# Performance work log

Hardware: AMD Instinct MI355X
Metric: run time of the kernel (lower is better)

Reference implementation:

```python
import jax, jax.numpy as jnp
import numpy as np

EPS_LEN = 1e-20
EPS_DENOM = 1e-6


def _dot(a, b):
    return jnp.sum(a * b, axis=-1, keepdims=True)


def _safe_normalize(x):
    return x / jnp.sqrt(jnp.maximum(_dot(x, x), EPS_LEN))


def _auto_normals(positions, faces):
    i0, i1, i2 = faces[:, 0], faces[:, 1], faces[:, 2]
    v0 = positions[i0]
    v1 = positions[i1]
    v2 = positions[i2]
    face_normals = jnp.cross(v1 - v0, v2 - v0)  # [F,3]
    v_nrm = jnp.zeros_like(positions)
    v_nrm = v_nrm.at[i0].add(face_normals)
    v_nrm = v_nrm.at[i1].add(face_normals)
    v_nrm = v_nrm.at[i2].add(face_normals)
    default = jnp.array([0.0, 0.0, 1.0], dtype=positions.dtype)
    v_nrm = jnp.where(_dot(v_nrm, v_nrm) > EPS_LEN, v_nrm, default)
    return _safe_normalize(v_nrm)


def _compute_tangents(positions, normals, faces, texcoords, uv_faces):
    pos = [positions[faces[:, i]] for i in range(3)]
    tex = [texcoords[uv_faces[:, i]] for i in range(3)]
    uve1 = tex[1] - tex[0]
    uve2 = tex[2] - tex[0]
    pe1 = pos[1] - pos[0]
    pe2 = pos[2] - pos[0]
    nom = pe1 * uve2[..., 1:2] - pe2 * uve1[..., 1:2]  # [F,3]
    denom = uve1[..., 0:1] * uve2[..., 1:2] - uve1[..., 1:2] * uve2[..., 0:1]
    denom = jnp.where(denom > 0.0,
                      jnp.maximum(denom, EPS_DENOM),
                      jnp.minimum(denom, -EPS_DENOM))
    tang = nom / denom  # [F,3]
    tangents = jnp.zeros_like(normals)
    for i in range(3):
        tangents = tangents.at[faces[:, i]].add(tang)
    tangents = _safe_normalize(tangents)
    tangents = _safe_normalize(tangents - _dot(tangents, normals) * normals)
    return tangents


def setup_inputs() -> dict:
    key = jax.random.key(0)
    k1, k2, k3, k4 = jax.random.split(key, 4)
    V, T, F = 2_000_000, 2_200_000, 4_000_000
    positions = jax.random.normal(k1, (V, 3), dtype=jnp.float32)
    faces = jax.random.randint(k2, (F, 3), 0, V, dtype=jnp.int32)
    texcoords = jax.random.uniform(k3, (T, 2), dtype=jnp.float32)
    uv_faces = jax.random.randint(k4, (F, 3), 0, T, dtype=jnp.int32)
    return {"positions": positions, "faces": faces,
            "texcoords": texcoords, "uv_faces": uv_faces}


def reference(positions, faces, texcoords, uv_faces):
    normals = _auto_normals(positions, faces)
    tangents = _compute_tangents(positions, normals, faces, texcoords, uv_faces)
    return jnp.stack([normals, tangents])  # [2, V, 3]
```

## Files before the change

### kernel.cpp

```cpp
#include <hip/hip_runtime.h>

#define EPS_LEN   1e-20f
#define EPS_DENOM 1e-6f

#define CB_LOG   11
#define CB       (1 << CB_LOG)
#define BLKA     1024
#define MAXB     1024
#define NCHUNK   2
#define CAPC     6528

#define CB2_LOG  13
#define CB2      (1 << CB2_LOG)
#define MAXB2    256
#define CAP2     57344
#define FST      6
#define QLOG     11
#define QSIZE    (1 << QLOG)

__global__ __launch_bounds__(BLKA)
void vg_face_bin_c(const float* __restrict__ pos, const int* __restrict__ faces,
                   const float* __restrict__ tex, const int* __restrict__ uvf,
                   float* __restrict__ en, float* __restrict__ et,
                   unsigned short* __restrict__ ev,
                   int* __restrict__ cursors, int* __restrict__ validw,
                   float* __restrict__ nacc, float* __restrict__ tacc,
                   int f0, int f1, int NBC)
{
    __shared__ int h[MAXB], sc[MAXB], loff[MAXB], lfill[MAXB], gbase[MAXB];
    __shared__ float spnx[BLKA], spny[BLKA], spnz[BLKA];
    __shared__ float sptx[BLKA], spty[BLKA], sptz[BLKA];
    __shared__ unsigned short sfl[3 * BLKA];
    __shared__ unsigned short svloc[3 * BLKA];
    __shared__ unsigned short sbuck[3 * BLKA];

    const int t = threadIdx.x;
    const int f = f0 + blockIdx.x * BLKA + t;

    h[t] = 0; lfill[t] = 0;
    for (int i = t; i < 3 * BLKA; i += BLKA) sbuck[i] = 0xFFFFu;
    __syncthreads();

    const bool on = (f < f1);
    int i0 = 0, i1 = 0, i2 = 0;
    float nx = 0, ny = 0, nz = 0, txv = 0, tyv = 0, tzv = 0;

    if (on) {
        i0 = faces[3 * f + 0]; i1 = faces[3 * f + 1]; i2 = faces[3 * f + 2];

        const float p0x = pos[3*i0+0], p0y = pos[3*i0+1], p0z = pos[3*i0+2];
        const float p1x = pos[3*i1+0], p1y = pos[3*i1+1], p1z = pos[3*i1+2];
        const float p2x = pos[3*i2+0], p2y = pos[3*i2+1], p2z = pos[3*i2+2];

        const float e1x = p1x - p0x, e1y = p1y - p0y, e1z = p1z - p0z;
        const float e2x = p2x - p0x, e2y = p2y - p0y, e2z = p2z - p0z;

        nx = e1y * e2z - e1z * e2y;
        ny = e1z * e2x - e1x * e2z;
        nz = e1x * e2y - e1y * e2x;

        const int t0 = uvf[3 * f + 0];
        const int t1 = uvf[3 * f + 1];
        const int t2 = uvf[3 * f + 2];

        const float u0x = tex[2*t0+0], u0y = tex[2*t0+1];
        const float u1x = tex[2*t1+0], u1y = tex[2*t1+1];
        const float u2x = tex[2*t2+0], u2y = tex[2*t2+1];

        const float d1x = u1x - u0x, d1y = u1y - u0y;
        const float d2x = u2x - u0x, d2y = u2y - u0y;

        float denom = d1x * d2y - d1y * d2x;
        denom = (denom > 0.0f) ? fmaxf(denom, EPS_DENOM) : fminf(denom, -EPS_DENOM);
        const float inv = 1.0f / denom;

        txv = (e1x * d2y - e2x * d1y) * inv;
        tyv = (e1y * d2y - e2y * d1y) * inv;
        tzv = (e1z * d2y - e2z * d1y) * inv;

        spnx[t] = nx;  spny[t] = ny;  spnz[t] = nz;
        sptx[t] = txv; spty[t] = tyv; sptz[t] = tzv;

        atomicAdd(&h[i0 >> CB_LOG], 1);
        atomicAdd(&h[i1 >> CB_LOG], 1);
        atomicAdd(&h[i2 >> CB_LOG], 1);
    }
    __syncthreads();

    sc[t] = h[t];
    __syncthreads();
    for (int d = 1; d < MAXB; d <<= 1) {
        const int v2 = sc[t] + ((t >= d) ? sc[t - d] : 0);
        __syncthreads();
        sc[t] = v2;
        __syncthreads();
    }
    {
        loff[t] = sc[t] - h[t];
        const int cnt = h[t];
        int gb = -1;
        if (t < NBC && cnt > 0) {
            gb = atomicAdd(&cursors[t], cnt);
            if (gb + cnt <= CAPC) atomicMax(&validw[t], gb + cnt);
            else gb = -1;
        }
        gbase[t] = gb;
    }
    __syncthreads();

    if (on) {
        const int vi[3] = { i0, i1, i2 };
#pragma unroll
        for (int c = 0; c < 3; ++c) {
            const int v = vi[c];
            const int b = v >> CB_LOG;
            if (gbase[b] >= 0) {
                const int slot = atomicAdd(&lfill[b], 1);
                const int p = loff[b] + slot;
                sfl[p]   = (unsigned short)t;
                svloc[p] = (unsigned short)(v & (CB - 1));
                sbuck[p] = (unsigned short)b;
            } else {
                atomicAdd(&nacc[3*v+0], nx);
                atomicAdd(&nacc[3*v+1], ny);
                atomicAdd(&nacc[3*v+2], nz);
                atomicAdd(&tacc[3*v+0], txv);
                atomicAdd(&tacc[3*v+1], tyv);
                atomicAdd(&tacc[3*v+2], tzv);
            }
        }
    }
    __syncthreads();

    for (int i = t; i < 3 * BLKA; i += BLKA) {
        const unsigned b = sbuck[i];
        if (b != 0xFFFFu) {
            const int g = gbase[b] + (i - loff[b]);
            const size_t s = (size_t)b * CAPC + g;
            const int fl = sfl[i];
            en[s*3+0] = spnx[fl]; en[s*3+1] = spny[fl]; en[s*3+2] = spnz[fl];
            et[s*3+0] = sptx[fl]; et[s*3+1] = spty[fl]; et[s*3+2] = sptz[fl];
            ev[s] = svloc[i];
        }
    }
}

__global__ __launch_bounds__(BLKA)
void vg_reduce_c(const float* __restrict__ en, const float* __restrict__ et,
                 const unsigned short* __restrict__ ev,
                 const int* __restrict__ validw,
                 float* __restrict__ nacc, float* __restrict__ tacc,
                 int V, int isFinal)
{
    __shared__ float accn[CB * 3];
    __shared__ float acct[CB * 3];
    const int b = blockIdx.x;
    const int t = threadIdx.x;

    for (int i = t; i < CB * 3; i += BLKA) { accn[i] = 0.0f; acct[i] = 0.0f; }
    __syncthreads();

    int count = validw[b];
    if (count > CAPC) count = CAPC;
    const size_t ebase = (size_t)b * CAPC;

    for (int e = t; e < count; e += BLKA) {
        const int vloc = (int)ev[ebase + e];
        const float* pn = &en[(ebase + e) * 3];
        const float* pt = &et[(ebase + e) * 3];
        float* an = &accn[vloc * 3];
        float* at = &acct[vloc * 3];
        atomicAdd(an + 0, pn[0]);
        atomicAdd(an + 1, pn[1]);
        atomicAdd(an + 2, pn[2]);
        atomicAdd(at + 0, pt[0]);
        atomicAdd(at + 1, pt[1]);
        atomicAdd(at + 2, pt[2]);
    }
    __syncthreads();

    const int vbase = b << CB_LOG;
#pragma unroll
    for (int k = 0; k < CB; k += BLKA) {
        const int i = t + k;
        const int v = vbase + i;
        if (v < V) {
            float nx = nacc[3*v+0] + accn[3*i+0];
            float ny = nacc[3*v+1] + accn[3*i+1];
            float nz = nacc[3*v+2] + accn[3*i+2];
            float tx = tacc[3*v+0] + acct[3*i+0];
            float ty = tacc[3*v+1] + acct[3*i+1];
            float tz = tacc[3*v+2] + acct[3*i+2];

            if (isFinal) {
                const float nd = nx*nx + ny*ny + nz*nz;
                if (nd > EPS_LEN) {
                    const float invn = 1.0f / sqrtf(nd);
                    nx *= invn; ny *= invn; nz *= invn;
                } else {
                    nx = 0.0f; ny = 0.0f; nz = 1.0f;
                }

                const float td = tx*tx + ty*ty + tz*tz;
                const float invt = 1.0f / sqrtf(fmaxf(td, EPS_LEN));
                tx *= invt; ty *= invt; tz *= invt;

                const float dp = tx*nx + ty*ny + tz*nz;
                tx -= dp * nx; ty -= dp * ny; tz -= dp * nz;

                const float td2 = tx*tx + ty*ty + tz*tz;
                const float invt2 = 1.0f / sqrtf(fmaxf(td2, EPS_LEN));
                tx *= invt2; ty *= invt2; tz *= invt2;
            }

            nacc[3*v+0] = nx; nacc[3*v+1] = ny; nacc[3*v+2] = nz;
            tacc[3*v+0] = tx; tacc[3*v+1] = ty; tacc[3*v+2] = tz;
        }
    }
}

__global__ __launch_bounds__(BLKA)
void vg_face_bin3(const float* __restrict__ pos, const int* __restrict__ faces,
                  const float* __restrict__ tex, const int* __restrict__ uvf,
                  float* __restrict__ face_data,
                  unsigned* __restrict__ ef, unsigned short* __restrict__ ev,
                  int* __restrict__ cursors, int* __restrict__ validw,
                  float* __restrict__ nacc, float* __restrict__ tacc,
                  int F, int NBC)
{
    __shared__ int h[MAXB2], sc[MAXB2], loff[MAXB2], lfill[MAXB2], gbase[MAXB2];
    __shared__ unsigned       sface[3 * BLKA];
    __shared__ unsigned short svloc[3 * BLKA];
    __shared__ unsigned char  sbuck[3 * BLKA];

    const int t = threadIdx.x;
    const int f = blockIdx.x * BLKA + t;

    if (t < MAXB2) { h[t] = 0; lfill[t] = 0; }
    for (int i = t; i < 3 * BLKA; i += BLKA) sbuck[i] = 0xFF;
    __syncthreads();

    const bool on = (f < F);
    int i0 = 0, i1 = 0, i2 = 0;
    float nx = 0, ny = 0, nz = 0, txv = 0, tyv = 0, tzv = 0;

    if (on) {
        i0 = faces[3 * f + 0]; i1 = faces[3 * f + 1]; i2 = faces[3 * f + 2];

        const float p0x = pos[3*i0+0], p0y = pos[3*i0+1], p0z = pos[3*i0+2];
        const float p1x = pos[3*i1+0], p1y = pos[3*i1+1], p1z = pos[3*i1+2];
        const float p2x = pos[3*i2+0], p2y = pos[3*i2+1], p2z = pos[3*i2+2];

        const float e1x = p1x - p0x, e1y = p1y - p0y, e1z = p1z - p0z;
        const float e2x = p2x - p0x, e2y = p2y - p0y, e2z = p2z - p0z;

        nx = e1y * e2z - e1z * e2y;
        ny = e1z * e2x - e1x * e2z;
        nz = e1x * e2y - e1y * e2x;

        const int t0 = uvf[3 * f + 0];
        const int t1 = uvf[3 * f + 1];
        const int t2 = uvf[3 * f + 2];

        const float u0x = tex[2*t0+0], u0y = tex[2*t0+1];
        const float u1x = tex[2*t1+0], u1y = tex[2*t1+1];
        const float u2x = tex[2*t2+0], u2y = tex[2*t2+1];

        const float d1x = u1x - u0x, d1y = u1y - u0y;
        const float d2x = u2x - u0x, d2y = u2y - u0y;

        float denom = d1x * d2y - d1y * d2x;
        denom = (denom > 0.0f) ? fmaxf(denom, EPS_DENOM) : fminf(denom, -EPS_DENOM);
        const float inv = 1.0f / denom;

        txv = (e1x * d2y - e2x * d1y) * inv;
        tyv = (e1y * d2y - e2y * d1y) * inv;
        tzv = (e1z * d2y - e2z * d1y) * inv;

        float* fd = &face_data[(size_t)f * FST];
        reinterpret_cast<float2*>(fd)[0] = make_float2(nx, ny);
        reinterpret_cast<float2*>(fd)[1] = make_float2(nz, txv);
        reinterpret_cast<float2*>(fd)[2] = make_float2(tyv, tzv);

        atomicAdd(&h[i0 >> CB2_LOG], 1);
        atomicAdd(&h[i1 >> CB2_LOG], 1);
        atomicAdd(&h[i2 >> CB2_LOG], 1);
    }
    __syncthreads();

    if (t < MAXB2) sc[t] = h[t];
    __syncthreads();
    for (int d = 1; d < MAXB2; d <<= 1) {
        int v2 = 0;
        if (t < MAXB2) v2 = sc[t] + ((t >= d) ? sc[t - d] : 0);
        __syncthreads();
        if (t < MAXB2) sc[t] = v2;
        __syncthreads();
    }
    if (t < MAXB2) {
        loff[t] = sc[t] - h[t];
        const int cnt = h[t];
        int gb = -1;
        if (t < NBC && cnt > 0) {
            gb = atomicAdd(&cursors[t], cnt);
            if (gb + cnt <= CAP2) atomicMax(&validw[t], gb + cnt);
            else gb = -1;
        }
        gbase[t] = gb;
    }
    __syncthreads();

    if (on) {
        const int vi[3] = { i0, i1, i2 };
#pragma unroll
        for (int c = 0; c < 3; ++c) {
            const int v = vi[c];
            const int b = v >> CB2_LOG;
            if (gbase[b] >= 0) {
                const int slot = atomicAdd(&lfill[b], 1);
                const int p = loff[b] + slot;
                sface[p] = (unsigned)f;
                svloc[p] = (unsigned short)(v & (CB2 - 1));
                sbuck[p] = (unsigned char)b;
            } else {
                atomicAdd(&nacc[3*v+0], nx);
                atomicAdd(&nacc[3*v+1], ny);
                atomicAdd(&nacc[3*v+2], nz);
                atomicAdd(&tacc[3*v+0], txv);
                atomicAdd(&tacc[3*v+1], tyv);
                atomicAdd(&tacc[3*v+2], tzv);
            }
        }
    }
    __syncthreads();

    for (int i = t; i < 3 * BLKA; i += BLKA) {
        const unsigned b = sbuck[i];
        if (b != 0xFFu) {
            const int g = gbase[b] + (i - loff[b]);
            const size_t base = (size_t)b * CAP2;
            ef[base + g] = sface[i];
            ev[base + g] = svloc[i];
        }
    }
}

__global__ __launch_bounds__(BLKA)
void vg_bucket_reduce3(const float* __restrict__ face_data,
                       const unsigned* __restrict__ ef,
                       const unsigned short* __restrict__ ev,
                       const int* __restrict__ validw,
                       float* __restrict__ nacc, float* __restrict__ tacc,
                       int V)
{
    __shared__ float acc[QSIZE * 6];
    const int b = blockIdx.x;
    const int t = threadIdx.x;
    int count = validw[b];
    if (count > CAP2) count = CAP2;
    const size_t ebase = (size_t)b * CAP2;
    const int vbase = b << CB2_LOG;

    for (int q = 0; q < 4; ++q) {
        for (int i = t; i < QSIZE * 6; i += BLKA) acc[i] = 0.0f;
        __syncthreads();

        for (int e = t; e < count; e += BLKA) {
            const int vloc = (int)ev[ebase + e];
            if ((vloc >> QLOG) == q) {
                const unsigned f = ef[ebase + e];
                const float* fd = &face_data[(size_t)f * FST];
                const float2 a0 = reinterpret_cast<const float2*>(fd)[0];
                const float2 a1 = reinterpret_cast<const float2*>(fd)[1];
                const float2 a2 = reinterpret_cast<const float2*>(fd)[2];
                float* a = &acc[(vloc & (QSIZE - 1)) * 6];
                atomicAdd(a + 0, a0.x);
                atomicAdd(a + 1, a0.y);
                atomicAdd(a + 2, a1.x);
                atomicAdd(a + 3, a1.y);
                atomicAdd(a + 4, a2.x);
                atomicAdd(a + 5, a2.y);
            }
        }
        __syncthreads();

        for (int i = t; i < QSIZE; i += BLKA) {
            const int v = vbase + (q << QLOG) + i;
            if (v < V) {
                float nx = nacc[3*v+0] + acc[i*6+0];
                float ny = nacc[3*v+1] + acc[i*6+1];
                float nz = nacc[3*v+2] + acc[i*6+2];
                float tx = tacc[3*v+0] + acc[i*6+3];
                float ty = tacc[3*v+1] + acc[i*6+4];
                float tz = tacc[3*v+2] + acc[i*6+5];

                const float nd = nx*nx + ny*ny + nz*nz;
                if (nd > EPS_LEN) {
                    const float invn = 1.0f / sqrtf(nd);
                    nx *= invn; ny *= invn; nz *= invn;
                } else {
                    nx = 0.0f; ny = 0.0f; nz = 1.0f;
                }

                const float td = tx*tx + ty*ty + tz*tz;
                const float invt = 1.0f / sqrtf(fmaxf(td, EPS_LEN));
                tx *= invt; ty *= invt; tz *= invt;

                const float dp = tx*nx + ty*ny + tz*nz;
                tx -= dp * nx; ty -= dp * ny; tz -= dp * nz;

                const float td2 = tx*tx + ty*ty + tz*tz;
                const float invt2 = 1.0f / sqrtf(fmaxf(td2, EPS_LEN));
                tx *= invt2; ty *= invt2; tz *= invt2;

                nacc[3*v+0] = nx; nacc[3*v+1] = ny; nacc[3*v+2] = nz;
                tacc[3*v+0] = tx; tacc[3*v+1] = ty; tacc[3*v+2] = tz;
            }
        }
        __syncthreads();
    }
}

__global__ void vg_face_kernel(const float* __restrict__ pos,
                               const int*   __restrict__ faces,
                               const float* __restrict__ tex,
                               const int*   __restrict__ uvf,
                               float* __restrict__ nacc,
                               float* __restrict__ tacc,
                               int F) {
    int f = blockIdx.x * blockDim.x + threadIdx.x;
    if (f >= F) return;

    const int i0 = faces[3*f+0], i1 = faces[3*f+1], i2 = faces[3*f+2];

    const float p0x = pos[3*i0+0], p0y = pos[3*i0+1], p0z = pos[3*i0+2];
    const float p1x = pos[3*i1+0], p1y = pos[3*i1+1], p1z = pos[3*i1+2];
    const float p2x = pos[3*i2+0], p2y = pos[3*i2+1], p2z = pos[3*i2+2];

    const float e1x = p1x - p0x, e1y = p1y - p0y, e1z = p1z - p0z;
    const float e2x = p2x - p0x, e2y = p2y - p0y, e2z = p2z - p0z;

    const float nx = e1y*e2z - e1z*e2y;
    const float ny = e1z*e2x - e1x*e2z;
    const float nz = e1x*e2y - e1y*e2x;

    const int t0 = uvf[3*f+0], t1 = uvf[3*f+1], t2 = uvf[3*f+2];

    const float u0x = tex[2*t0+0], u0y = tex[2*t0+1];
    const float u1x = tex[2*t1+0], u1y = tex[2*t1+1];
    const float u2x = tex[2*t2+0], u2y = tex[2*t2+1];

    const float d1x = u1x - u0x, d1y = u1y - u0y;
    const float d2x = u2x - u0x, d2y = u2y - u0y;

    float denom = d1x * d2y - d1y * d2x;
    denom = (denom > 0.0f) ? fmaxf(denom, EPS_DENOM) : fminf(denom, -EPS_DENOM);
    const float inv = 1.0f / denom;

    const float tx = (e1x*d2y - e2x*d1y) * inv;
    const float ty = (e1y*d2y - e2y*d1y) * inv;
    const float tz = (e1z*d2y - e2z*d1y) * inv;

    atomicAdd(&nacc[3*i0+0], nx); atomicAdd(&nacc[3*i0+1], ny); atomicAdd(&nacc[3*i0+2], nz);
    atomicAdd(&nacc[3*i1+0], nx); atomicAdd(&nacc[3*i1+1], ny); atomicAdd(&nacc[3*i1+2], nz);
    atomicAdd(&nacc[3*i2+0], nx); atomicAdd(&nacc[3*i2+1], ny); atomicAdd(&nacc[3*i2+2], nz);
    atomicAdd(&tacc[3*i0+0], tx); atomicAdd(&tacc[3*i0+1], ty); atomicAdd(&tacc[3*i0+2], tz);
    atomicAdd(&tacc[3*i1+0], tx); atomicAdd(&tacc[3*i1+1], ty); atomicAdd(&tacc[3*i1+2], tz);
    atomicAdd(&tacc[3*i2+0], tx); atomicAdd(&tacc[3*i2+1], ty); atomicAdd(&tacc[3*i2+2], tz);
}

__global__ void vg_finalize_kernel(float* __restrict__ nacc,
                                   float* __restrict__ tacc,
                                   int V) {
    int v = blockIdx.x * blockDim.x + threadIdx.x;
    if (v >= V) return;

    float nx = nacc[3*v+0], ny = nacc[3*v+1], nz = nacc[3*v+2];
    float nd = nx*nx + ny*ny + nz*nz;
    if (nd > EPS_LEN) {
        const float invn = 1.0f / sqrtf(nd);
        nx *= invn; ny *= invn; nz *= invn;
    } else {
        nx = 0.0f; ny = 0.0f; nz = 1.0f;
    }

    float tx = tacc[3*v+0], ty = tacc[3*v+1], tz = tacc[3*v+2];
    float td = tx*tx + ty*ty + tz*tz;
    float invt = 1.0f / sqrtf(fmaxf(td, EPS_LEN));
    tx *= invt; ty *= invt; tz *= invt;
    const float dp = tx*nx + ty*ny + tz*nz;
    tx -= dp*nx; ty -= dp*ny; tz -= dp*nz;
    float td2 = tx*tx + ty*ty + tz*tz;
    float invt2 = 1.0f / sqrtf(fmaxf(td2, EPS_LEN));
    tx *= invt2; ty *= invt2; tz *= invt2;

    nacc[3*v+0] = nx; nacc[3*v+1] = ny; nacc[3*v+2] = nz;
    tacc[3*v+0] = tx; tacc[3*v+1] = ty; tacc[3*v+2] = tz;
}

extern "C" void kernel_launch(void* const* d_in, const int* in_sizes, int n_in,
                              void* d_out, int out_size, void* d_ws, size_t ws_size,
                              hipStream_t stream) {
    const float* pos   = (const float*)d_in[0];
    const int*   faces = (const int*)  d_in[1];
    const float* tex   = (const float*)d_in[2];
    const int*   uvf   = (const int*)  d_in[3];

    const int V = in_sizes[0] / 3;
    const int F = in_sizes[1] / 3;

    float* out  = (float*)d_out;
    float* nacc = out;
    float* tacc = out + (size_t)3 * V;

    hipMemsetAsync(d_out, 0, (size_t)out_size * sizeof(float), stream);

    const int NBC1 = (V + CB - 1) >> CB_LOG;
    {
        const size_t NE1   = (size_t)NBC1 * CAPC;
        const size_t en_b  = (NE1 * 12 + 255) & ~(size_t)255;
        const size_t et_b  = (NE1 * 12 + 255) & ~(size_t)255;
        const size_t ev_b  = (NE1 * 2 + 255) & ~(size_t)255;
        const size_t cur_b = ((size_t)NBC1 * sizeof(int) + 255) & ~(size_t)255;
        const size_t need1 = en_b + et_b + ev_b + 2 * cur_b + 256;

        if (ws_size >= need1 && NBC1 <= MAXB) {
            char* ws = (char*)d_ws;
            float*          en  = (float*)ws;          ws += en_b;
            float*          et  = (float*)ws;          ws += et_b;
            unsigned short* ev  = (unsigned short*)ws; ws += ev_b;
            int*            cursors = (int*)ws;        ws += cur_b;
            int*            validw  = (int*)ws;

            const int Fc = (F + NCHUNK - 1) / NCHUNK;
            for (int c = 0; c < NCHUNK; ++c) {
                const int f0 = c * Fc;
                const int f1 = (f0 + Fc < F) ? (f0 + Fc) : F;
                if (f0 >= f1) continue;

                hipMemsetAsync(cursors, 0, cur_b, stream);
                hipMemsetAsync(validw,  0, cur_b, stream);

                const int nblk = (f1 - f0 + BLKA - 1) / BLKA;
                vg_face_bin_c<<<nblk, BLKA, 0, stream>>>(
                    pos, faces, tex, uvf, en, et, ev, cursors, validw,
                    nacc, tacc, f0, f1, NBC1);

                const int isFinal = (f1 == F) ? 1 : 0;
                vg_reduce_c<<<NBC1, BLKA, 0, stream>>>(
                    en, et, ev, validw, nacc, tacc, V, isFinal);
            }
            return;
        }
    }

    const int NBC2 = (V + CB2 - 1) >> CB2_LOG;
    {
        const size_t NE2    = (size_t)NBC2 * CAP2;
        const size_t face_b = ((size_t)F * FST * sizeof(float) + 255) & ~(size_t)255;
        const size_t ef_b   = (NE2 * 4 + 255) & ~(size_t)255;
        const size_t ev2_b  = (NE2 * 2 + 255) & ~(size_t)255;
        const size_t cur_b  = ((size_t)NBC2 * sizeof(int) + 255) & ~(size_t)255;
        const size_t need2  = face_b + ef_b + ev2_b + 2 * cur_b + 256;

        if (ws_size >= need2 && NBC2 <= 255 && F < (1 << 22)) {
            char* ws = (char*)d_ws;
            float*          face_data = (float*)ws;          ws += face_b;
            unsigned*       ef        = (unsigned*)ws;       ws += ef_b;
            unsigned short* ev        = (unsigned short*)ws; ws += ev2_b;
            int*            cursors   = (int*)ws;            ws += cur_b;
            int*            validw    = (int*)ws;

            hipMemsetAsync(cursors, 0, cur_b, stream);
            hipMemsetAsync(validw,  0, cur_b, stream);

            vg_face_bin3<<<(F + BLKA - 1) / BLKA, BLKA, 0, stream>>>(
                pos, faces, tex, uvf, face_data, ef, ev, cursors, validw,
                nacc, tacc, F, NBC2);
            vg_bucket_reduce3<<<NBC2, BLKA, 0, stream>>>(
                face_data, ef, ev, validw, nacc, tacc, V);
            return;
        }
    }

    const int BLK = 256;
    vg_face_kernel<<<(F + BLK - 1) / BLK, BLK, 0, stream>>>(pos, faces, tex, uvf,
                                                            nacc, tacc, F);
    vg_finalize_kernel<<<(V + BLK - 1) / BLK, BLK, 0, stream>>>(nacc, tacc, V);
}
```

Baseline: 1.067 ms.

## Bin face indices instead of face payloads and gather per-bucket in reduce

Measured after the change: 920.1 us. -13.7%, faster.

```diff
diff --git a/kernel.cpp b/kernel.cpp
--- a/kernel.cpp
+++ b/kernel.cpp
@@ -3,45 +3,45 @@
 #define EPS_LEN   1e-20f
 #define EPS_DENOM 1e-6f
 
-#define CB_LOG   11
-#define CB       (1 << CB_LOG)
 #define BLKA     1024
-#define MAXB     1024
-#define NCHUNK   2
-#define CAPC     6528
+
+#define CBF_LOG  10
+#define CBF      (1 << CBF_LOG)
+#define NBCP     2048
+#define CAPF     7168
+#define FST      6
 
 #define CB2_LOG  13
 #define CB2      (1 << CB2_LOG)
 #define MAXB2    256
 #define CAP2     57344
-#define FST      6
 #define QLOG     11
 #define QSIZE    (1 << QLOG)
 
 __global__ __launch_bounds__(BLKA)
-void vg_face_bin_c(const float* __restrict__ pos, const int* __restrict__ faces,
+void vg_face_bin_f(const float* __restrict__ pos, const int* __restrict__ faces,
                    const float* __restrict__ tex, const int* __restrict__ uvf,
-                   float* __restrict__ en, float* __restrict__ et,
-                   unsigned short* __restrict__ ev,
+                   float* __restrict__ face_data, unsigned* __restrict__ E,
                    int* __restrict__ cursors, int* __restrict__ validw,
                    float* __restrict__ nacc, float* __restrict__ tacc,
-                   int f0, int f1, int NBC)
+                   int F, int NBC)
 {
-    __shared__ int h[MAXB], sc[MAXB], loff[MAXB], lfill[MAXB], gbase[MAXB];
-    __shared__ float spnx[BLKA], spny[BLKA], spnz[BLKA];
-    __shared__ float sptx[BLKA], spty[BLKA], sptz[BLKA];
-    __shared__ unsigned short sfl[3 * BLKA];
-    __shared__ unsigned short svloc[3 * BLKA];
+    __shared__ int h[NBCP];
+    __shared__ int s0[NBCP];
+    __shared__ int s1[NBCP];
+    __shared__ int lfill[NBCP];
+    __shared__ unsigned       spack[3 * BLKA];
     __shared__ unsigned short sbuck[3 * BLKA];
 
     const int t = threadIdx.x;
-    const int f = f0 + blockIdx.x * BLKA + t;
-
-    h[t] = 0; lfill[t] = 0;
+    const int f = blockIdx.x * BLKA + t;
+
+    h[t] = 0; h[t + 1024] = 0;
+    lfill[t] = 0; lfill[t + 1024] = 0;
     for (int i = t; i < 3 * BLKA; i += BLKA) sbuck[i] = 0xFFFFu;
     __syncthreads();
 
-    const bool on = (f < f1);
+    const bool on = (f < F);
     int i0 = 0, i1 = 0, i2 = 0;
     float nx = 0, ny = 0, nz = 0, txv = 0, tyv = 0, tzv = 0;
 
@@ -78,33 +78,41 @@
         tyv = (e1y * d2y - e2y * d1y) * inv;
         tzv = (e1z * d2y - e2z * d1y) * inv;
 
-        spnx[t] = nx;  spny[t] = ny;  spnz[t] = nz;
-        sptx[t] = txv; spty[t] = tyv; sptz[t] = tzv;
-
-        atomicAdd(&h[i0 >> CB_LOG], 1);
-        atomicAdd(&h[i1 >> CB_LOG], 1);
-        atomicAdd(&h[i2 >> CB_LOG], 1);
-    }
-    __syncthreads();
-
-    sc[t] = h[t];
-    __syncthreads();
-    for (int d = 1; d < MAXB; d <<= 1) {
-        const int v2 = sc[t] + ((t >= d) ? sc[t - d] : 0);
+        float* fd = &face_data[(size_t)f * FST];
+        reinterpret_cast<float2*>(fd)[0] = make_float2(nx, ny);
+        reinterpret_cast<float2*>(fd)[1] = make_float2(nz, txv);
+        reinterpret_cast<float2*>(fd)[2] = make_float2(tyv, tzv);
+
+        atomicAdd(&h[i0 >> CBF_LOG], 1);
+        atomicAdd(&h[i1 >> CBF_LOG], 1);
+        atomicAdd(&h[i2 >> CBF_LOG], 1);
+    }
+    __syncthreads();
+
+    s0[t] = h[t]; s0[t + 1024] = h[t + 1024];
+    __syncthreads();
+    int* src = s0; int* dst = s1;
+    for (int d = 1; d < NBCP; d <<= 1) {
+        dst[t] = src[t] + ((t >= d) ? src[t - d] : 0);
+        const int k = t + 1024;
+        dst[k] = src[k] + ((k >= d) ? src[k - d] : 0);
         __syncthreads();
-        sc[t] = v2;
-        __syncthreads();
-    }
-    {
-        loff[t] = sc[t] - h[t];
-        const int cnt = h[t];
+        int* tmp = src; src = dst; dst = tmp;
+    }
+    int* loffp  = dst;
+    int* gbasep = h;
+    for (int k = t; k < NBCP; k += 1024) {
+        const int incl = src[k];
+        const int cnt  = h[k];
+        const int lo   = incl - cnt;
         int gb = -1;
-        if (t < NBC && cnt > 0) {
-            gb = atomicAdd(&cursors[t], cnt);
-            if (gb + cnt <= CAPC) atomicMax(&validw[t], gb + cnt);
+        if (k < NBC && cnt > 0) {
+            gb = atomicAdd(&cursors[k], cnt);
+            if (gb + cnt <= CAPF) atomicMax(&validw[k], gb + cnt);
             else gb = -1;
         }
-        gbase[t] = gb;
+        loffp[k]  = lo;
+        gbasep[k] = gb;
     }
     __syncthreads();
 
@@ -113,12 +121,11 @@
 #pragma unroll
         for (int c = 0; c < 3; ++c) {
             const int v = vi[c];
-            const int b = v >> CB_LOG;
-            if (gbase[b] >= 0) {
+            const int b = v >> CBF_LOG;
+            if (gbasep[b] >= 0) {
                 const int slot = atomicAdd(&lfill[b], 1);
-                const int p = loff[b] + slot;
-                sfl[p]   = (unsigned short)t;
-                svloc[p] = (unsigned short)(v & (CB - 1));
+                const int p = loffp[b] + slot;
+                spack[p] = ((unsigned)(v & (CBF - 1)) << 22) | (unsigned)f;
                 sbuck[p] = (unsigned short)b;
             } else {
                 atomicAdd(&nacc[3*v+0], nx);
@@ -135,53 +142,53 @@
     for (int i = t; i < 3 * BLKA; i += BLKA) {
         const unsigned b = sbuck[i];
         if (b != 0xFFFFu) {
-            const int g = gbase[b] + (i - loff[b]);
-            const size_t s = (size_t)b * CAPC + g;
-            const int fl = sfl[i];
-            en[s*3+0] = spnx[fl]; en[s*3+1] = spny[fl]; en[s*3+2] = spnz[fl];
-            et[s*3+0] = sptx[fl]; et[s*3+1] = spty[fl]; et[s*3+2] = sptz[fl];
-            ev[s] = svloc[i];
-        }
-    }
-}
-
-__global__ __launch_bounds__(BLKA)
-void vg_reduce_c(const float* __restrict__ en, const float* __restrict__ et,
-                 const unsigned short* __restrict__ ev,
-                 const int* __restrict__ validw,
-                 float* __restrict__ nacc, float* __restrict__ tacc,
-                 int V, int isFinal)
+            const int g = gbasep[b] + (i - loffp[b]);
+            E[(size_t)b * CAPF + g] = spack[i];
+        }
+    }
+}
+
+__global__ __launch_bounds__(512)
+void vg_gather_reduce_f(const float* __restrict__ face_data,
+                        const unsigned* __restrict__ E,
+                        const int* __restrict__ validw,
+                        float* __restrict__ nacc, float* __restrict__ tacc,
+                        int V)
 {
-    __shared__ float accn[CB * 3];
-    __shared__ float acct[CB * 3];
+    __shared__ float accn[CBF * 3];
+    __shared__ float acct[CBF * 3];
     const int b = blockIdx.x;
     const int t = threadIdx.x;
 
-    for (int i = t; i < CB * 3; i += BLKA) { accn[i] = 0.0f; acct[i] = 0.0f; }
+    for (int i = t; i < CBF * 3; i += 512) { accn[i] = 0.0f; acct[i] = 0.0f; }
     __syncthreads();
 
     int count = validw[b];
-    if (count > CAPC) count = CAPC;
-    const size_t ebase = (size_t)b * CAPC;
-
-    for (int e = t; e < count; e += BLKA) {
-        const int vloc = (int)ev[ebase + e];
-        const float* pn = &en[(ebase + e) * 3];
-        const float* pt = &et[(ebase + e) * 3];
+    if (count > CAPF) count = CAPF;
+    const size_t ebase = (size_t)b * CAPF;
+
+    for (int e = t; e < count; e += 512) {
+        const unsigned ent = E[ebase + e];
+        const int f    = (int)(ent & 0x3FFFFFu);
+        const int vloc = (int)(ent >> 22);
+        const float* fd = &face_data[(size_t)f * FST];
+        const float2 a0 = reinterpret_cast<const float2*>(fd)[0];
+        const float2 a1 = reinterpret_cast<const float2*>(fd)[1];
+        const float2 a2 = reinterpret_cast<const float2*>(fd)[2];
         float* an = &accn[vloc * 3];
         float* at = &acct[vloc * 3];
-        atomicAdd(an + 0, pn[0]);
-        atomicAdd(an + 1, pn[1]);
-        atomicAdd(an + 2, pn[2]);
-        atomicAdd(at + 0, pt[0]);
-        atomicAdd(at + 1, pt[1]);
-        atomicAdd(at + 2, pt[2]);
-    }
-    __syncthreads();
-
-    const int vbase = b << CB_LOG;
+        atomicAdd(an + 0, a0.x);
+        atomicAdd(an + 1, a0.y);
+        atomicAdd(an + 2, a1.x);
+        atomicAdd(at + 0, a1.y);
+        atomicAdd(at + 1, a2.x);
+        atomicAdd(at + 2, a2.y);
+    }
+    __syncthreads();
+
+    const int vbase = b << CBF_LOG;
 #pragma unroll
-    for (int k = 0; k < CB; k += BLKA) {
+    for (int k = 0; k < CBF; k += 512) {
         const int i = t + k;
         const int v = vbase + i;
         if (v < V) {
@@ -192,26 +199,24 @@
             float ty = tacc[3*v+1] + acct[3*i+1];
             float tz = tacc[3*v+2] + acct[3*i+2];
 
-            if (isFinal) {
-                const float nd = nx*nx + ny*ny + nz*nz;
-                if (nd > EPS_LEN) {
-                    const float invn = 1.0f / sqrtf(nd);
-                    nx *= invn; ny *= invn; nz *= invn;
-                } else {
-                    nx = 0.0f; ny = 0.0f; nz = 1.0f;
-                }
-
-                const float td = tx*tx + ty*ty + tz*tz;
-                const float invt = 1.0f / sqrtf(fmaxf(td, EPS_LEN));
-                tx *= invt; ty *= invt; tz *= invt;
-
-                const float dp = tx*nx + ty*ny + tz*nz;
-                tx -= dp * nx; ty -= dp * ny; tz -= dp * nz;
-
-                const float td2 = tx*tx + ty*ty + tz*tz;
-                const float invt2 = 1.0f / sqrtf(fmaxf(td2, EPS_LEN));
-                tx *= invt2; ty *= invt2; tz *= invt2;
+            const float nd = nx*nx + ny*ny + nz*nz;
+            if (nd > EPS_LEN) {
+                const float invn = 1.0f / sqrtf(nd);
+                nx *= invn; ny *= invn; nz *= invn;
+            } else {
+                nx = 0.0f; ny = 0.0f; nz = 1.0f;
             }
+
+            const float td = tx*tx + ty*ty + tz*tz;
+            const float invt = 1.0f / sqrtf(fmaxf(td, EPS_LEN));
+            tx *= invt; ty *= invt; tz *= invt;
+
+            const float dp = tx*nx + ty*ny + tz*nz;
+            tx -= dp * nx; ty -= dp * ny; tz -= dp * nz;
+
+            const float td2 = tx*tx + ty*ty + tz*tz;
+            const float invt2 = 1.0f / sqrtf(fmaxf(td2, EPS_LEN));
+            tx *= invt2; ty *= invt2; tz *= invt2;
 
             nacc[3*v+0] = nx; nacc[3*v+1] = ny; nacc[3*v+2] = nz;
             tacc[3*v+0] = tx; tacc[3*v+1] = ty; tacc[3*v+2] = tz;
@@ -515,41 +520,28 @@
 
     hipMemsetAsync(d_out, 0, (size_t)out_size * sizeof(float), stream);
 
-    const int NBC1 = (V + CB - 1) >> CB_LOG;
+    const int NBC1 = (V + CBF - 1) >> CBF_LOG;
     {
-        const size_t NE1   = (size_t)NBC1 * CAPC;
-        const size_t en_b  = (NE1 * 12 + 255) & ~(size_t)255;
-        const size_t et_b  = (NE1 * 12 + 255) & ~(size_t)255;
-        const size_t ev_b  = (NE1 * 2 + 255) & ~(size_t)255;
-        const size_t cur_b = ((size_t)NBC1 * sizeof(int) + 255) & ~(size_t)255;
-        const size_t need1 = en_b + et_b + ev_b + 2 * cur_b + 256;
-
-        if (ws_size >= need1 && NBC1 <= MAXB) {
+        const size_t face_b = ((size_t)F * FST * sizeof(float) + 255) & ~(size_t)255;
+        const size_t E_b    = ((size_t)NBC1 * CAPF * sizeof(unsigned) + 255) & ~(size_t)255;
+        const size_t cur_b  = ((size_t)NBC1 * sizeof(int) + 255) & ~(size_t)255;
+        const size_t need1  = face_b + E_b + 2 * cur_b + 256;
+
+        if (ws_size >= need1 && NBC1 <= NBCP && F <= (1 << 22)) {
             char* ws = (char*)d_ws;
-            float*          en  = (float*)ws;          ws += en_b;
-            float*          et  = (float*)ws;          ws += et_b;
-            unsigned short* ev  = (unsigned short*)ws; ws += ev_b;
-            int*            cursors = (int*)ws;        ws += cur_b;
-            int*            validw  = (int*)ws;
-
-            const int Fc = (F + NCHUNK - 1) / NCHUNK;
-            for (int c = 0; c < NCHUNK; ++c) {
-                const int f0 = c * Fc;
-                const int f1 = (f0 + Fc < F) ? (f0 + Fc) : F;
-                if (f0 >= f1) continue;
-
-                hipMemsetAsync(cursors, 0, cur_b, stream);
-                hipMemsetAsync(validw,  0, cur_b, stream);
-
-                const int nblk = (f1 - f0 + BLKA - 1) / BLKA;
-                vg_face_bin_c<<<nblk, BLKA, 0, stream>>>(
-                    pos, faces, tex, uvf, en, et, ev, cursors, validw,
-                    nacc, tacc, f0, f1, NBC1);
-
-                const int isFinal = (f1 == F) ? 1 : 0;
-                vg_reduce_c<<<NBC1, BLKA, 0, stream>>>(
-                    en, et, ev, validw, nacc, tacc, V, isFinal);
-            }
+            float*    face_data = (float*)ws;    ws += face_b;
+            unsigned* E         = (unsigned*)ws; ws += E_b;
+            int*      cursors   = (int*)ws;      ws += cur_b;
+            int*      validw    = (int*)ws;
+
+            hipMemsetAsync(cursors, 0, cur_b, stream);
+            hipMemsetAsync(validw,  0, cur_b, stream);
+
+            vg_face_bin_f<<<(F + BLKA - 1) / BLKA, BLKA, 0, stream>>>(
+                pos, faces, tex, uvf, face_data, E, cursors, validw,
+                nacc, tacc, F, NBC1);
+            vg_gather_reduce_f<<<NBC1, 512, 0, stream>>>(
+                face_data, E, validw, nacc, tacc, V);
             return;
         }
     }
```
